# Kernel tuning notes

Measured on AMD Instinct MI355X. Metric: run time of the kernel, lower is better.

## Reference

```python
import jax, jax.numpy as jnp
import numpy as np

GRID = 24          # grid_size = sqrt(N-1)
N = GRID * GRID + 1
C = 768
H = 12
D = C // H
WINDOW = 7
B = 32


def build_local_mask(seq_len, grid_size, window_size):
    # patch (row, col) coordinates for tokens 1..N-1
    idx = np.arange(seq_len - 1)
    row = idx // grid_size
    col = idx % grid_size
    r = window_size // 2
    # local window: |dr| <= r and |dc| <= r (matches the torch double loop)
    patch_mask = (np.abs(row[:, None] - row[None, :]) <= r) & \
                 (np.abs(col[:, None] - col[None, :]) <= r)
    mask = np.zeros((seq_len, seq_len), dtype=bool)
    mask[1:, 1:] = patch_mask
    mask[0, :] = True   # CLS attends to all
    mask[:, 0] = True   # all attend to CLS
    return jnp.asarray(mask)


def setup_inputs() -> dict:
    key = jax.random.key(0)
    kx, kqkv, kproj = jax.random.split(key, 3)
    x = jax.random.normal(kx, (B, N, C), dtype=jnp.float32)
    W_qkv = jax.random.normal(kqkv, (C, 3 * C), dtype=jnp.float32) * 0.02
    W_proj = jax.random.normal(kproj, (C, C), dtype=jnp.float32) * 0.02
    b_proj = jnp.zeros((C,), dtype=jnp.float32)
    mask = build_local_mask(N, GRID, WINDOW)
    return {"x": x, "W_qkv": W_qkv, "W_proj": W_proj, "b_proj": b_proj, "mask": mask}


def reference(x, W_qkv, W_proj, b_proj, mask):
    Bb, Nn, Cc = x.shape
    scale = 1.0 / jnp.sqrt(jnp.asarray(D, dtype=x.dtype))
    qkv = (x @ W_qkv).reshape(Bb, Nn, 3, H, D)
    qkv = jnp.transpose(qkv, (2, 0, 3, 1, 4))  # [3, B, H, N, D]
    q, k, v = qkv[0], qkv[1], qkv[2]
    attn = jnp.einsum('bhnd,bhmd->bhnm', q, k) * scale
    attn = jnp.where(mask[None, None, :, :], attn, jnp.asarray(-jnp.inf, dtype=attn.dtype))
    attn = jax.nn.softmax(attn, axis=-1)
    out = jnp.einsum('bhnm,bhmd->bhnd', attn, v)  # [B, H, N, D]
    out = jnp.transpose(out, (0, 2, 1, 3)).reshape(Bb, Nn, Cc)
    return out @ W_proj + b_proj
```

## Files before the change

### kernel.cpp

```cpp
#include <hip/hip_runtime.h>
#include <stdint.h>

#define GRID_S 24
#define NTOK   577
#define CDIM   768
#define HEADS  12
#define DHEAD  64
#define BATCH  32

#define MREAL  (BATCH*NTOK)
#define MTILES 145
#define MPAD   (MTILES*128)
#define KDIM   768
#define NQKV   2304
#define VTP    584

typedef __attribute__((ext_vector_type(4))) float         f32x4;
typedef __attribute__((ext_vector_type(8))) short         s16x8;
typedef __attribute__((ext_vector_type(4))) unsigned int  u32x4;
typedef __attribute__((address_space(1))) const void g_void;
typedef __attribute__((address_space(3))) void lds_void;

__device__ __forceinline__ unsigned short f2bf(float f) {
    unsigned int u = __float_as_uint(f);
    u += 0x7fffu + ((u >> 16) & 1u);
    return (unsigned short)(u >> 16);
}
__device__ __forceinline__ float bf2f(unsigned short h) {
    return __uint_as_float(((unsigned int)h) << 16);
}

extern "C" __global__ void __launch_bounds__(256)
k_cast_x(const float* __restrict__ x, unsigned short* __restrict__ xb) {
    const long long n4 = (long long)MPAD * CDIM / 4;
    const long long v4 = (long long)MREAL * CDIM / 4;
    long long i = (long long)blockIdx.x * blockDim.x + threadIdx.x;
    const long long stride = (long long)gridDim.x * blockDim.x;
    for (; i < n4; i += stride) {
        float4 v = (i < v4) ? ((const float4*)x)[i] : make_float4(0.f, 0.f, 0.f, 0.f);
        ushort4 o;
        o.x = f2bf(v.x); o.y = f2bf(v.y); o.z = f2bf(v.z); o.w = f2bf(v.w);
        ((ushort4*)xb)[i] = o;
    }
}

extern "C" __global__ void __launch_bounds__(256)
k_tcast(const float* __restrict__ W, unsigned short* __restrict__ WT, int ncol, int n) {
    int i = blockIdx.x * blockDim.x + threadIdx.x;
    const int stride = gridDim.x * blockDim.x;
    for (; i < n; i += stride) {
        const int c = i / KDIM;
        const int k = i - c * KDIM;
        WT[i] = f2bf(W[(long long)k * ncol + c]);
    }
}

__device__ __forceinline__ void gemm_core(const unsigned short* __restrict__ A,
                                          const unsigned short* __restrict__ BT,
                                          int m0, int n0,
                                          unsigned short* As, unsigned short* Bs,
                                          f32x4 acc[4][4]) {
    const int tid  = threadIdx.x;
    const int lane = tid & 63;
    const int wid  = tid >> 6;
    const int wm = wid >> 1, wn = wid & 1;
    const int lrow = lane & 15;
    const int kh   = (lane >> 4) * 8;
    const int srow = (lane >> 2);
    const int scol = (lane & 3) * 16;

#pragma unroll
    for (int i = 0; i < 4; i++)
#pragma unroll
        for (int j = 0; j < 4; j++)
            acc[i][j] = (f32x4){0.f, 0.f, 0.f, 0.f};

#define STAGE(buf, k0) { _Pragma("unroll")                                             \
    for (int c = 0; c < 2; ++c) {                                                      \
        const int chunk = wid * 2 + c;                               \
        const int row   = chunk * 16 + srow;                                           \
        const char* ga = (const char*)(A  + (long long)(m0 + row) * KDIM + (k0)) + scol; \
        const char* gb = (const char*)(BT + (long long)(n0 + row) * KDIM + (k0)) + scol; \
        __builtin_amdgcn_global_load_lds((g_void*)ga, (lds_void*)((char*)As + (buf) * 8192 + chunk * 1024), 16, 0, 0); \
        __builtin_amdgcn_global_load_lds((g_void*)gb, (lds_void*)((char*)Bs + (buf) * 8192 + chunk * 1024), 16, 0, 0); \
    } }

    STAGE(0, 0)
    __syncthreads();

    for (int step = 0; step < KDIM / 32; ++step) {
        const int buf = step & 1;
        if (step + 1 < KDIM / 32) STAGE(buf ^ 1, (step + 1) * 32)

        const unsigned short* Ab = As + buf * 4096;
        const unsigned short* Bb = Bs + buf * 4096;
        s16x8 af[4], bq[4];
#pragma unroll
        for (int f = 0; f < 4; ++f) {
            af[f] = *(const s16x8*)(Ab + (wm * 64 + f * 16 + lrow) * 32 + kh);
            bq[f] = *(const s16x8*)(Bb + (wn * 64 + f * 16 + lrow) * 32 + kh);
        }
#pragma unroll
        for (int i = 0; i < 4; i++)
#pragma unroll
            for (int j = 0; j < 4; j++)
                acc[i][j] = __builtin_amdgcn_mfma_f32_16x16x32_bf16(af[i], bq[j], acc[i][j], 0, 0, 0);
        __syncthreads();
    }
#undef STAGE
}

extern "C" __global__ void __launch_bounds__(256)
k_gemm_qkv(const unsigned short* __restrict__ A, const unsigned short* __restrict__ BT,
           unsigned short* __restrict__ Qb, unsigned short* __restrict__ Kb,
           unsigned short* __restrict__ Vb) {
    __shared__ unsigned short As[2 * 128 * 32];
    __shared__ unsigned short Bs[2 * 128 * 32];
    const int m0 = blockIdx.x * 128;
    const int n0 = blockIdx.y * 128;
    f32x4 acc[4][4];
    gemm_core(A, BT, m0, n0, As, Bs, acc);

    const int lane = threadIdx.x & 63;
    const int wid  = threadIdx.x >> 6;
    const int wm = wid >> 1, wn = wid & 1;
    const int lrow = lane & 15;
#pragma unroll
    for (int fi = 0; fi < 4; ++fi) {
        const int mbase = m0 + wm * 64 + fi * 16 + (lane >> 4) * 4;
#pragma unroll
        for (int fj = 0; fj < 4; ++fj) {
            const int cb  = n0 + wn * 64 + fj * 16;
            const int s   = cb / 768;
            const int rem = cb - s * 768;
            const int h   = rem >> 6;
            const int d   = (rem & 63) + lrow;
            const float sc = (s == 0) ? 0.125f : 1.0f;
            unsigned short* dst = (s == 0) ? Qb : (s == 1) ? Kb : Vb;
#pragma unroll
            for (int i = 0; i < 4; i++) {
                const int m = mbase + i;
                if (m < MREAL) {
                    const int b  = m / NTOK;
                    const int nn = m - b * NTOK;
                    dst[(((long long)(b * HEADS + h)) * NTOK + nn) * DHEAD + d] = f2bf(acc[fi][fj][i] * sc);
                }
            }
        }
    }
}

extern "C" __global__ void __launch_bounds__(256)
k_gemm_proj(const unsigned short* __restrict__ A, const unsigned short* __restrict__ BT,
            const float* __restrict__ bias, float* __restrict__ out) {
    __shared__ unsigned short As[2 * 128 * 32];
    __shared__ unsigned short Bs[2 * 128 * 32];
    const int m0 = blockIdx.x * 128;
    const int n0 = blockIdx.y * 128;
    f32x4 acc[4][4];
    gemm_core(A, BT, m0, n0, As, Bs, acc);

    const int lane = threadIdx.x & 63;
    const int wid  = threadIdx.x >> 6;
    const int wm = wid >> 1, wn = wid & 1;
    const int lrow = lane & 15;
#pragma unroll
    for (int fi = 0; fi < 4; ++fi) {
        const int mbase = m0 + wm * 64 + fi * 16 + (lane >> 4) * 4;
#pragma unroll
        for (int fj = 0; fj < 4; ++fj) {
            const int col = n0 + wn * 64 + fj * 16 + lrow;
            const float bv = bias[col];
#pragma unroll
            for (int i = 0; i < 4; i++) {
                const int m = mbase + i;
                if (m < MREAL) out[(long long)m * CDIM + col] = acc[fi][fj][i] + bv;
            }
        }
    }
}

extern "C" __global__ void __launch_bounds__(256)
k_vtrans(const unsigned short* __restrict__ Vb, unsigned short* __restrict__ Vt) {
    __shared__ unsigned short S[64 * 66];
    const int bh = blockIdx.x;
    const int n0 = 1 + blockIdx.y * 64;
    const int t  = threadIdx.x;
    {
        const int tr = t >> 2, cq = t & 3;
        const unsigned short* src = Vb + ((long long)bh * NTOK + n0 + tr) * 64 + cq * 16;
        ushort4 a0 = *(const ushort4*)(src + 0);
        ushort4 a1 = *(const ushort4*)(src + 4);
        ushort4 a2 = *(const ushort4*)(src + 8);
        ushort4 a3 = *(const ushort4*)(src + 12);
        unsigned short* dl = S + tr * 66 + cq * 16;
        dl[0]=a0.x; dl[1]=a0.y; dl[2]=a0.z; dl[3]=a0.w;
        dl[4]=a1.x; dl[5]=a1.y; dl[6]=a1.z; dl[7]=a1.w;
        dl[8]=a2.x; dl[9]=a2.y; dl[10]=a2.z; dl[11]=a2.w;
        dl[12]=a3.x; dl[13]=a3.y; dl[14]=a3.z; dl[15]=a3.w;
    }
    __syncthreads();
    {
        const int dr = t >> 2, tq = t & 3;
        unsigned short o[16];
#pragma unroll
        for (int j = 0; j < 16; ++j) o[j] = S[(tq * 16 + j) * 66 + dr];
        unsigned short* dst = Vt + ((long long)bh * 64 + dr) * VTP + (n0 - 1) + tq * 16;
#pragma unroll
        for (int j = 0; j < 16; ++j) dst[j] = o[j];
    }
}

extern "C" __global__ void __launch_bounds__(256)
k_attn2(const unsigned short* __restrict__ Qb, const unsigned short* __restrict__ Kb,
        const unsigned short* __restrict__ Vb, const unsigned short* __restrict__ Vt,
        unsigned short* __restrict__ AO) {
    const int l   = threadIdx.x & 63;
    const int w   = threadIdx.x >> 6;
    const int bh  = blockIdx.x;
    const int qt  = blockIdx.y;
    const int qbase = qt * 64 + w * 16;
    if (qbase >= NTOK) return;
    const int q15 = l & 15;
    const int hi  = l >> 4;
    const int kh  = hi * 8;

    const unsigned short* Qh  = Qb + (long long)bh * NTOK * 64;
    const unsigned short* Kh  = Kb + (long long)bh * NTOK * 64;
    const unsigned short* Vbh = Vb + (long long)bh * NTOK * 64;
    const unsigned short* Vh  = Vt + (long long)bh * 64 * VTP;

    const int qn_frag = min(qbase + q15, NTOK - 1);
    const s16x8 qf0 = *(const s16x8*)(Qh + (long long)qn_frag * 64 + kh);
    const s16x8 qf1 = *(const s16x8*)(Qh + (long long)qn_frag * 64 + 32 + kh);

    const int q_n = qbase + q15;
    const bool q_is_cls = (q_n == 0);
    int pr = 0, pc = 0;
    {
        const int p = (q_n >= 1 ? min(q_n, NTOK - 1) : 1) - 1;
        pr = p / GRID_S; pc = p - pr * GRID_S;
    }

    int ks, ke;
    if (qbase == 0) { ks = 1; ke = NTOK; }
    else {
        const int nlo = qbase, nhi = min(qbase + 15, NTOK - 1);
        const int prmin = (nlo - 1) / GRID_S, prmax = (nhi - 1) / GRID_S;
        const int rlo = max(0, prmin - 3), rhi = min(GRID_S - 1, prmax + 3);
        ks = 1 + rlo * GRID_S; ke = 1 + (rhi + 1) * GRID_S;
    }

    float s0 = 0.f;
    {
        const s16x8 k0a = *(const s16x8*)(Kh + kh);
        const s16x8 k0b = *(const s16x8*)(Kh + 32 + kh);
#pragma unroll
        for (int j = 0; j < 8; ++j) {
            s0 += bf2f((unsigned short)qf0[j]) * bf2f((unsigned short)k0a[j]);
            s0 += bf2f((unsigned short)qf1[j]) * bf2f((unsigned short)k0b[j]);
        }
    }
    s0 += __shfl_xor(s0, 16, 64);
    s0 += __shfl_xor(s0, 32, 64);
    const float e0 = __expf(s0);

    float e0q[4];
#pragma unroll
    for (int i = 0; i < 4; ++i) e0q[i] = __shfl(e0, (hi << 2) + i, 64);

    f32x4 Oacc[4];
#pragma unroll
    for (int dt = 0; dt < 4; ++dt) {
        const float v0 = bf2f(Vbh[dt * 16 + q15]);
        f32x4 t; t[0] = e0q[0]*v0; t[1] = e0q[1]*v0; t[2] = e0q[2]*v0; t[3] = e0q[3]*v0;
        Oacc[dt] = t;
    }

    float dsum = 0.f;
    const int nch = (ke - ks + 31) >> 5;
    for (int ch = 0; ch < nch; ++ch) {
        const int cb = ks + (ch << 5);
        f32x4 ct0 = (f32x4){0,0,0,0}, ct1 = (f32x4){0,0,0,0};

#define QK_TILE(TB, CT) {                                                          \
            const int key = min((TB) + q15, NTOK - 1);                             \
            const unsigned short* kp_ = Kh + (long long)key * 64 + kh;             \
            const s16x8 ka  = *(const s16x8*)kp_;                                  \
            const s16x8 kb2 = *(const s16x8*)(kp_ + 32);                           \
            f32x4 c = __builtin_amdgcn_mfma_f32_16x16x32_bf16(ka,  qf0, (f32x4){0,0,0,0}, 0,0,0); \
            c = __builtin_amdgcn_mfma_f32_16x16x32_bf16(kb2, qf1, c, 0,0,0);       \
            _Pragma("unroll")                                                      \
            for (int i = 0; i < 4; ++i) {                                          \
                const int kk  = (TB) + (hi << 2) + i;                              \
                const int kpp = kk - 1;                                            \
                const int kr  = kpp / GRID_S;                                      \
                const int kc  = kpp - kr * GRID_S;                                 \
                const bool win = ((unsigned)(kr - pr + 3) <= 6u) && ((unsigned)(kc - pc + 3) <= 6u); \
                const bool valid = (kk < ke) && (q_is_cls || win);                 \
                const float e = valid ? __expf(c[i]) : 0.f;                        \
                CT[i] = e; dsum += e;                                              \
            } }

        QK_TILE(cb, ct0)
        if (cb + 16 < ke) QK_TILE(cb + 16, ct1)
#undef QK_TILE

        float pv[8];
#pragma unroll
        for (int j = 0; j < 8; ++j) {
            const int src = ((((hi & 1) << 3) + j) >> 2) * 16 + q15;
            const float a0 = __shfl(ct0[j & 3], src, 64);
            const float a1 = __shfl(ct1[j & 3], src, 64);
            pv[j] = (hi & 2) ? a1 : a0;
        }
        u32x4 paw;
#pragma unroll
        for (int t = 0; t < 4; ++t)
            paw[t] = (unsigned)f2bf(pv[2 * t]) | ((unsigned)f2bf(pv[2 * t + 1]) << 16);
        const s16x8 pa16 = __builtin_bit_cast(s16x8, paw);

        const int gvb = cb - 1 + kh;
#pragma unroll
        for (int dt = 0; dt < 4; ++dt) {
            const s16x8 vf = *(const s16x8*)(Vh + (long long)(dt * 16 + q15) * VTP + gvb);
            Oacc[dt] = __builtin_amdgcn_mfma_f32_16x16x32_bf16(pa16, vf, Oacc[dt], 0, 0, 0);
        }
    }

    dsum += __shfl_xor(dsum, 16, 64);
    dsum += __shfl_xor(dsum, 32, 64);
    const float tot = e0 + dsum;
    float rq[4];
#pragma unroll
    for (int i = 0; i < 4; ++i) rq[i] = 1.f / __shfl(tot, (hi << 2) + i, 64);

    const int b = bh / HEADS, h = bh - b * HEADS;
#pragma unroll
    for (int i = 0; i < 4; ++i) {
        const int n = qbase + (hi << 2) + i;
        if (n < NTOK) {
#pragma unroll
            for (int dt = 0; dt < 4; ++dt)
                AO[((long long)(b * NTOK + n)) * CDIM + h * 64 + dt * 16 + q15] =
                    f2bf(Oacc[dt][i] * rq[i]);
        }
    }
}

extern "C" void kernel_launch(void* const* d_in, const int* in_sizes, int n_in,
                              void* d_out, int out_size, void* d_ws, size_t ws_size,
                              hipStream_t stream) {
    (void)in_sizes; (void)n_in; (void)out_size; (void)ws_size;
    const float* x     = (const float*)d_in[0];
    const float* Wqkv  = (const float*)d_in[1];
    const float* Wproj = (const float*)d_in[2];
    const float* bproj = (const float*)d_in[3];
    float* out = (float*)d_out;
    char*  ws  = (char*)d_ws;

    unsigned short* xb  = (unsigned short*)(ws);
    unsigned short* wqT = (unsigned short*)(ws + 28508160LL);
    unsigned short* wpT = (unsigned short*)(ws + 32047104LL);
    unsigned short* Qb  = (unsigned short*)(ws + 33226752LL);
    unsigned short* Kb  = (unsigned short*)(ws + 61593600LL);
    unsigned short* Vb  = (unsigned short*)(ws + 89960448LL);
    unsigned short* AO  = (unsigned short*)(ws + 118327296LL);
    unsigned short* Vt  = (unsigned short*)(ws);

    hipLaunchKernelGGL(k_cast_x,  dim3(2048), dim3(256), 0, stream, x, xb);
    hipLaunchKernelGGL(k_tcast,   dim3(2048), dim3(256), 0, stream, Wqkv, wqT, NQKV, KDIM * NQKV);
    hipLaunchKernelGGL(k_tcast,   dim3(1024), dim3(256), 0, stream, Wproj, wpT, CDIM, KDIM * CDIM);
    hipLaunchKernelGGL(k_gemm_qkv, dim3(MTILES, NQKV / 128), dim3(256), 0, stream, xb, wqT, Qb, Kb, Vb);
    hipLaunchKernelGGL(k_vtrans,  dim3(384, 9), dim3(256), 0, stream, Vb, Vt);
    hipLaunchKernelGGL(k_attn2,   dim3(384, 10), dim3(256), 0, stream, Qb, Kb, Vb, Vt, AO);
    hipLaunchKernelGGL(k_gemm_proj, dim3(MTILES, CDIM / 128), dim3(256), 0, stream, AO, wpT, bproj, out);
}
```

Baseline: 382.0 us.

## Add XCD-aware workgroup swizzle to GEMMs and drop LDS double buffering

Both GEMM kernels now launch a 1D grid and remap block IDs so each XCD gets a contiguous chunk of tiles, with m-major ordering so neighbouring tiles share A rows and B columns in that XCD's L2. The GEMM core also switches from double-buffered LDS staging to a single buffer that is loaded and synced before compute in each k-step. This halves LDS use per block, which may allow more resident blocks, but it removes the overlap of global loads with MFMA work.

```diff
diff --git a/kernel.cpp b/kernel.cpp
--- a/kernel.cpp
+++ b/kernel.cpp
@@ -28,6 +28,12 @@
 }
 __device__ __forceinline__ float bf2f(unsigned short h) {
     return __uint_as_float(((unsigned int)h) << 16);
+}
+
+__device__ __forceinline__ int xcd_chunk_swizzle(int orig, int nwg) {
+    const int q = nwg >> 3, r = nwg & 7;
+    const int xcd = orig & 7, off = orig >> 3;
+    return (xcd < r ? xcd * (q + 1) : r * (q + 1) + (xcd - r) * q) + off;
 }
 
 extern "C" __global__ void __launch_bounds__(256)
@@ -75,30 +81,23 @@
         for (int j = 0; j < 4; j++)
             acc[i][j] = (f32x4){0.f, 0.f, 0.f, 0.f};
 
-#define STAGE(buf, k0) { _Pragma("unroll")                                             \
-    for (int c = 0; c < 2; ++c) {                                                      \
-        const int chunk = wid * 2 + c;                               \
-        const int row   = chunk * 16 + srow;                                           \
-        const char* ga = (const char*)(A  + (long long)(m0 + row) * KDIM + (k0)) + scol; \
-        const char* gb = (const char*)(BT + (long long)(n0 + row) * KDIM + (k0)) + scol; \
-        __builtin_amdgcn_global_load_lds((g_void*)ga, (lds_void*)((char*)As + (buf) * 8192 + chunk * 1024), 16, 0, 0); \
-        __builtin_amdgcn_global_load_lds((g_void*)gb, (lds_void*)((char*)Bs + (buf) * 8192 + chunk * 1024), 16, 0, 0); \
-    } }
-
-    STAGE(0, 0)
-    __syncthreads();
-
-    for (int step = 0; step < KDIM / 32; ++step) {
-        const int buf = step & 1;
-        if (step + 1 < KDIM / 32) STAGE(buf ^ 1, (step + 1) * 32)
-
-        const unsigned short* Ab = As + buf * 4096;
-        const unsigned short* Bb = Bs + buf * 4096;
+    for (int k0 = 0; k0 < KDIM; k0 += 32) {
+#pragma unroll
+        for (int c = 0; c < 2; ++c) {
+            const int chunk = wid * 2 + c;
+            const int row   = chunk * 16 + srow;
+            const char* ga = (const char*)(A  + (long long)(m0 + row) * KDIM + k0) + scol;
+            const char* gb = (const char*)(BT + (long long)(n0 + row) * KDIM + k0) + scol;
+            __builtin_amdgcn_global_load_lds((g_void*)ga, (lds_void*)((char*)As + chunk * 1024), 16, 0, 0);
+            __builtin_amdgcn_global_load_lds((g_void*)gb, (lds_void*)((char*)Bs + chunk * 1024), 16, 0, 0);
+        }
+        __syncthreads();
+
         s16x8 af[4], bq[4];
 #pragma unroll
         for (int f = 0; f < 4; ++f) {
-            af[f] = *(const s16x8*)(Ab + (wm * 64 + f * 16 + lrow) * 32 + kh);
-            bq[f] = *(const s16x8*)(Bb + (wn * 64 + f * 16 + lrow) * 32 + kh);
+            af[f] = *(const s16x8*)(As + (wm * 64 + f * 16 + lrow) * 32 + kh);
+            bq[f] = *(const s16x8*)(Bs + (wn * 64 + f * 16 + lrow) * 32 + kh);
         }
 #pragma unroll
         for (int i = 0; i < 4; i++)
@@ -107,17 +106,19 @@
                 acc[i][j] = __builtin_amdgcn_mfma_f32_16x16x32_bf16(af[i], bq[j], acc[i][j], 0, 0, 0);
         __syncthreads();
     }
-#undef STAGE
-}
-
+}
+
+#define QKV_NT (NQKV/128)
+#define QKV_NWG (MTILES*QKV_NT)
 extern "C" __global__ void __launch_bounds__(256)
 k_gemm_qkv(const unsigned short* __restrict__ A, const unsigned short* __restrict__ BT,
            unsigned short* __restrict__ Qb, unsigned short* __restrict__ Kb,
            unsigned short* __restrict__ Vb) {
-    __shared__ unsigned short As[2 * 128 * 32];
-    __shared__ unsigned short Bs[2 * 128 * 32];
-    const int m0 = blockIdx.x * 128;
-    const int n0 = blockIdx.y * 128;
+    __shared__ unsigned short As[128 * 32];
+    __shared__ unsigned short Bs[128 * 32];
+    const int wgid = xcd_chunk_swizzle(blockIdx.x, QKV_NWG);
+    const int m0 = (wgid / QKV_NT) * 128;
+    const int n0 = (wgid % QKV_NT) * 128;
     f32x4 acc[4][4];
     gemm_core(A, BT, m0, n0, As, Bs, acc);
 
@@ -150,13 +151,16 @@
     }
 }
 
+#define PROJ_NT (CDIM/128)
+#define PROJ_NWG (MTILES*PROJ_NT)
 extern "C" __global__ void __launch_bounds__(256)
 k_gemm_proj(const unsigned short* __restrict__ A, const unsigned short* __restrict__ BT,
             const float* __restrict__ bias, float* __restrict__ out) {
-    __shared__ unsigned short As[2 * 128 * 32];
-    __shared__ unsigned short Bs[2 * 128 * 32];
-    const int m0 = blockIdx.x * 128;
-    const int n0 = blockIdx.y * 128;
+    __shared__ unsigned short As[128 * 32];
+    __shared__ unsigned short Bs[128 * 32];
+    const int wgid = xcd_chunk_swizzle(blockIdx.x, PROJ_NWG);
+    const int m0 = (wgid / PROJ_NT) * 128;
+    const int n0 = (wgid % PROJ_NT) * 128;
     f32x4 acc[4][4];
     gemm_core(A, BT, m0, n0, As, Bs, acc);
 
@@ -371,8 +375,8 @@
     hipLaunchKernelGGL(k_cast_x,  dim3(2048), dim3(256), 0, stream, x, xb);
     hipLaunchKernelGGL(k_tcast,   dim3(2048), dim3(256), 0, stream, Wqkv, wqT, NQKV, KDIM * NQKV);
     hipLaunchKernelGGL(k_tcast,   dim3(1024), dim3(256), 0, stream, Wproj, wpT, CDIM, KDIM * CDIM);
-    hipLaunchKernelGGL(k_gemm_qkv, dim3(MTILES, NQKV / 128), dim3(256), 0, stream, xb, wqT, Qb, Kb, Vb);
+    hipLaunchKernelGGL(k_gemm_qkv, dim3(QKV_NWG), dim3(256), 0, stream, xb, wqT, Qb, Kb, Vb);
     hipLaunchKernelGGL(k_vtrans,  dim3(384, 9), dim3(256), 0, stream, Vb, Vt);
     hipLaunchKernelGGL(k_attn2,   dim3(384, 10), dim3(256), 0, stream, Qb, Kb, Vb, Vt, AO);
-    hipLaunchKernelGGL(k_gemm_proj, dim3(MTILES, CDIM / 128), dim3(256), 0, stream, AO, wpT, bproj, out);
-}
+    hipLaunchKernelGGL(k_gemm_proj, dim3(PROJ_NWG), dim3(256), 0, stream, AO, wpT, bproj, out);
+}
```

After: 356.7 us. 6.6% less time.
